# Optimization experiments

Measured on AMD Instinct MI355X. Metric: run time of the kernel, lower is better.

Reference implementation:

```python
import jax, jax.numpy as jnp
import numpy as np

V, H, B = 64, 128, 16384  # num_visible, num_hidden = alpha*V, batch of spin configs
ISCALE = 0.001


def setup_inputs() -> dict:
    key = jax.random.key(0)
    k1, k2, k3, k4 = jax.random.split(key, 4)
    x = jax.random.normal(k1, (B, V), dtype=jnp.float32)
    weight_1 = jax.random.normal(k2, (V, H), dtype=jnp.float32) * ISCALE
    weight_2 = jax.random.normal(k3, (H, V, V), dtype=jnp.float32) * (ISCALE / 10.0)
    hidden_bias = jax.random.normal(k4, (H,), dtype=jnp.float32) * ISCALE
    return {"x": x, "weight_1": weight_1, "weight_2": weight_2, "hidden_bias": hidden_bias}


def reference(x, weight_1, weight_2, hidden_bias):
    b, v = x.shape
    h = weight_2.shape[0]
    # order-1 term: (B,V) @ (V,H) -> (B,H)
    w1 = x @ weight_1
    # order-2 term: outer product of spins per sample, contracted with weight_2.
    # vis_ij: (B,V,V) flattened to (B,V*V); weight_2 flattened to (H,V*V) -> GEMM.
    vis_ij = jnp.einsum('mi,mj->mij', x, x).reshape(b, v * v)
    w2 = (vis_ij @ weight_2.reshape(h, v * v).T) * 0.5
    act = jnp.cos(hidden_bias + w1 + w2)  # (B,H)
    psi = jnp.prod(act, axis=-1)          # (B,)
    return psi
```

## Files before the change

### kernel.cpp

```cpp
#include <hip/hip_runtime.h>
#include <hip/hip_bf16.h>
#include <cstdint>

#define NV 64
#define NH 128
#define NB 16384
#define W2_ELEMS (NH * NV * NV)
#define W1_ELEMS (NV * NH)

typedef __bf16 bf16x8_t __attribute__((ext_vector_type(8)));
typedef float f32x4_t __attribute__((ext_vector_type(4)));
typedef float f32x2_t __attribute__((ext_vector_type(2)));
typedef uint32_t u32x4_t __attribute__((ext_vector_type(4)));
typedef uint32_t u32x2_t __attribute__((ext_vector_type(2)));

__device__ __forceinline__ uint32_t bf16_rne(float f) {
  uint32_t u = __float_as_uint(f);
  return (u + 0x7fffu + ((u >> 16) & 1u)) >> 16;
}

__global__ void cvt_kernel(const float* __restrict__ w1f,
                           const float* __restrict__ w2f,
                           uint16_t* __restrict__ wsW2,
                           uint16_t* __restrict__ wsW1t) {
  int base = (blockIdx.x * 256 + threadIdx.x) * 4;
  if (base < W2_ELEMS) {
    float4 v = *(const float4*)(w2f + base);
    uint2 p;
    p.x = (bf16_rne(0.5f * v.y) << 16) | bf16_rne(0.5f * v.x);
    p.y = (bf16_rne(0.5f * v.w) << 16) | bf16_rne(0.5f * v.z);
    *(uint2*)(wsW2 + base) = p;
  } else {
    int off = base - W2_ELEMS;
    float4 v = *(const float4*)(w1f + off);
    const float d[4] = {v.x, v.y, v.z, v.w};
#pragma unroll
    for (int e = 0; e < 4; ++e) {
      int idx = off + e;
      int j = idx >> 7, h = idx & 127;
      wsW1t[h * 64 + j] = (uint16_t)bf16_rne(d[e]);
    }
  }
}

__launch_bounds__(512, 2)
__global__ void rbm_kernel(const float* __restrict__ xg,
                           const float* __restrict__ biasg,
                           const __hip_bfloat16* __restrict__ w1tg,
                           const __hip_bfloat16* __restrict__ w2g,
                           float* __restrict__ outg) {
  __shared__ __align__(16) __hip_bfloat16 btile[2][NH * 64];
  __shared__ __align__(16) float xtile[64 * 68];
  __shared__ float part[4][64];

  const int tid  = threadIdx.x;
  const int wv   = tid >> 6;
  const int lane = tid & 63;
  const int c15  = lane & 15;
  const int q    = lane >> 4;
  const int wm   = wv & 1;
  const int hq   = wv >> 1;
  const int mblk = blockIdx.x * 64;

  const int sh = tid >> 2;
  const int g0 = tid & 3, g1 = g0 + 4;
  const __hip_bfloat16* w2row = w2g + (size_t)sh * 4096;
  const int d0 = sh * 64 + ((g0 ^ (sh & 7)) * 8);
  const int d1 = sh * 64 + ((g1 ^ (sh & 7)) * 8);

  {
    int row = tid >> 3, grp = tid & 7;
    const float* p = xg + (size_t)(mblk + row) * NV + grp * 8;
    float4 a = *(const float4*)(p);
    float4 b = *(const float4*)(p + 4);
    *(float4*)(&xtile[row * 68 + grp * 8]) = a;
    *(float4*)(&xtile[row * 68 + grp * 8 + 4]) = b;
  }

  f32x2_t xf[2][2][4];
#pragma unroll
  for (int im = 0; im < 2; ++im) {
    int row = mblk + 32 * wm + 16 * im + c15;
#pragma unroll
    for (int jh = 0; jh < 2; ++jh) {
      const float* p = xg + (size_t)row * NV + jh * 32 + q * 8;
      float4 a = *(const float4*)(p);
      float4 b = *(const float4*)(p + 4);
      xf[im][jh][0] = f32x2_t{a.x, a.y};
      xf[im][jh][1] = f32x2_t{a.z, a.w};
      xf[im][jh][2] = f32x2_t{b.x, b.y};
      xf[im][jh][3] = f32x2_t{b.z, b.w};
    }
  }

  int boff[2][2];
#pragma unroll
  for (int ih = 0; ih < 2; ++ih) {
    int hrow = 32 * hq + 16 * ih + c15;
#pragma unroll
    for (int jh = 0; jh < 2; ++jh)
      boff[ih][jh] = hrow * 64 + (((jh * 4 + q) ^ (hrow & 7)) * 8);
  }

  {
    uint4 p0 = *(const uint4*)(w2row + g0 * 8);
    uint4 p1 = *(const uint4*)(w2row + g1 * 8);
    *(uint4*)(&btile[0][d0]) = p0;
    *(uint4*)(&btile[0][d1]) = p1;
  }
  __syncthreads();

  f32x4_t acc[2][2];
#pragma unroll
  for (int im = 0; im < 2; ++im)
#pragma unroll
    for (int ih = 0; ih < 2; ++ih)
      acc[im][ih] = (f32x4_t)0.0f;

#pragma unroll 2
  for (int c = 0; c < 64; ++c) {
    const int buf = c & 1;
    uint4 p0, p1;
    if (c < 63) {
      const __hip_bfloat16* src = w2row + (c + 1) * 64;
      p0 = *(const uint4*)(src + g0 * 8);
      p1 = *(const uint4*)(src + g1 * 8);
    }
    float s[2];
#pragma unroll
    for (int im = 0; im < 2; ++im)
      s[im] = xtile[(32 * wm + 16 * im + c15) * 68 + c];

#pragma unroll
    for (int jh = 0; jh < 2; ++jh) {
      bf16x8_t afrag[2];
#pragma unroll
      for (int im = 0; im < 2; ++im) {
        const f32x2_t s2 = f32x2_t{s[im], s[im]};
        u32x4_t adv;
#pragma unroll
        for (int t = 0; t < 4; ++t) {
          f32x2_t pr = s2 * xf[im][jh][t];
          u32x2_t u = __builtin_bit_cast(u32x2_t, pr);
          adv[t] = __builtin_amdgcn_perm(u[1], u[0], 0x07060302);
        }
        afrag[im] = __builtin_bit_cast(bf16x8_t, adv);
      }
#pragma unroll
      for (int ih = 0; ih < 2; ++ih) {
        bf16x8_t bfrag = *(const bf16x8_t*)(&btile[buf][boff[ih][jh]]);
#pragma unroll
        for (int im = 0; im < 2; ++im)
          acc[im][ih] = __builtin_amdgcn_mfma_f32_16x16x32_bf16(
              afrag[im], bfrag, acc[im][ih], 0, 0, 0);
      }
    }
    if (c < 63) {
      *(uint4*)(&btile[buf ^ 1][d0]) = p0;
      *(uint4*)(&btile[buf ^ 1][d1]) = p1;
      __syncthreads();
    }
  }

#pragma unroll
  for (int cc = 0; cc < 2; ++cc) {
    bf16x8_t afrag[2];
#pragma unroll
    for (int im = 0; im < 2; ++im) {
      u32x4_t adv;
#pragma unroll
      for (int t = 0; t < 4; ++t) {
        u32x2_t u = __builtin_bit_cast(u32x2_t, xf[im][cc][t]);
        adv[t] = __builtin_amdgcn_perm(u[1], u[0], 0x07060302);
      }
      afrag[im] = __builtin_bit_cast(bf16x8_t, adv);
    }
#pragma unroll
    for (int ih = 0; ih < 2; ++ih) {
      int hrow = 32 * hq + 16 * ih + c15;
      bf16x8_t bfrag = *(const bf16x8_t*)(w1tg + hrow * 64 + cc * 32 + q * 8);
#pragma unroll
      for (int im = 0; im < 2; ++im)
        acc[im][ih] = __builtin_amdgcn_mfma_f32_16x16x32_bf16(
            afrag[im], bfrag, acc[im][ih], 0, 0, 0);
    }
  }

  float bs[2];
#pragma unroll
  for (int ih = 0; ih < 2; ++ih)
    bs[ih] = biasg[32 * hq + 16 * ih + c15];

  float prod[2][4];
#pragma unroll
  for (int im = 0; im < 2; ++im)
#pragma unroll
    for (int r = 0; r < 4; ++r)
      prod[im][r] = cosf(acc[im][0][r] + bs[0]) * cosf(acc[im][1][r] + bs[1]);

#pragma unroll
  for (int ofs = 1; ofs < 16; ofs <<= 1)
#pragma unroll
    for (int im = 0; im < 2; ++im)
#pragma unroll
      for (int r = 0; r < 4; ++r)
        prod[im][r] *= __shfl_xor(prod[im][r], ofs, 16);

  if (c15 == 0) {
#pragma unroll
    for (int im = 0; im < 2; ++im)
#pragma unroll
      for (int r = 0; r < 4; ++r)
        part[hq][32 * wm + 16 * im + 4 * q + r] = prod[im][r];
  }
  __syncthreads();
  if (tid < 64) {
    float f = part[0][tid] * part[1][tid] * part[2][tid] * part[3][tid];
    outg[mblk + tid] = f;
  }
}

extern "C" void kernel_launch(void* const* d_in, const int* in_sizes, int n_in,
                              void* d_out, int out_size, void* d_ws, size_t ws_size,
                              hipStream_t stream) {
  const float* x   = (const float*)d_in[0];
  const float* w1f = (const float*)d_in[1];
  const float* w2f = (const float*)d_in[2];
  const float* hb  = (const float*)d_in[3];
  float* out = (float*)d_out;
  uint16_t* wsW2  = (uint16_t*)d_ws;
  uint16_t* wsW1t = wsW2 + W2_ELEMS;
  (void)in_sizes; (void)n_in; (void)out_size; (void)ws_size;

  cvt_kernel<<<(W2_ELEMS + W1_ELEMS) / (256 * 4), 256, 0, stream>>>(
      w1f, w2f, wsW2, wsW1t);
  rbm_kernel<<<NB / 64, 512, 0, stream>>>(
      x, hb, (const __hip_bfloat16*)wsW1t, (const __hip_bfloat16*)wsW2, out);
}
```

Measured before the change: 99.64 us.

## Pre-swizzle weights into MFMA fragment layout and stream B directly from global

The weight conversion kernel now writes W2 and transposed W1 in the exact per-lane MFMA B-fragment order, so the main kernel loads B fragments straight from global/L2 into registers with a one-step register prefetch. This removes the LDS double-buffer and its per-iteration barrier. W1 is folded into the loop as a 65th chunk by setting an extra x column to 1. Blocks shrink to 4 waves, each covering all 64 rows against 32 hidden units, which doubles A-fragment reuse per B load. Cosine switches to the hardware sin/cos instruction with a 1/2π scale, trading accuracy for speed.

```diff
diff --git a/kernel.cpp b/kernel.cpp
--- a/kernel.cpp
+++ b/kernel.cpp
@@ -5,8 +5,7 @@
 #define NV 64
 #define NH 128
 #define NB 16384
-#define W2_ELEMS (NH * NV * NV)
-#define W1_ELEMS (NV * NH)
+#define FRAG_ELEMS (130 * 8 * 512)
 
 typedef __bf16 bf16x8_t __attribute__((ext_vector_type(8)));
 typedef float f32x4_t __attribute__((ext_vector_type(4)));
@@ -21,71 +20,77 @@
 
 __global__ void cvt_kernel(const float* __restrict__ w1f,
                            const float* __restrict__ w2f,
-                           uint16_t* __restrict__ wsW2,
-                           uint16_t* __restrict__ wsW1t) {
-  int base = (blockIdx.x * 256 + threadIdx.x) * 4;
-  if (base < W2_ELEMS) {
-    float4 v = *(const float4*)(w2f + base);
-    uint2 p;
-    p.x = (bf16_rne(0.5f * v.y) << 16) | bf16_rne(0.5f * v.x);
-    p.y = (bf16_rne(0.5f * v.w) << 16) | bf16_rne(0.5f * v.z);
-    *(uint2*)(wsW2 + base) = p;
+                           uint16_t* __restrict__ frag) {
+  int tg = blockIdx.x * 256 + threadIdx.x;
+  if (tg < 128 * 512) {
+    int h = tg >> 9, k8 = tg & 511;
+    const float* p = w2f + ((size_t)h << 12) + k8 * 8;
+    float4 a = *(const float4*)p;
+    float4 b = *(const float4*)(p + 4);
+    uint4 o;
+    o.x = (bf16_rne(0.5f * a.y) << 16) | bf16_rne(0.5f * a.x);
+    o.y = (bf16_rne(0.5f * a.w) << 16) | bf16_rne(0.5f * a.z);
+    o.z = (bf16_rne(0.5f * b.y) << 16) | bf16_rne(0.5f * b.x);
+    o.w = (bf16_rne(0.5f * b.w) << 16) | bf16_rne(0.5f * b.z);
+    int c2 = k8 >> 2, lhi = k8 & 3;
+    int fh = h >> 4, l = lhi * 16 + (h & 15);
+    *(uint4*)(frag + (((c2 * 8 + fh) * 64 + l) << 3)) = o;
   } else {
-    int off = base - W2_ELEMS;
-    float4 v = *(const float4*)(w1f + off);
-    const float d[4] = {v.x, v.y, v.z, v.w};
-#pragma unroll
-    for (int e = 0; e < 4; ++e) {
-      int idx = off + e;
-      int j = idx >> 7, h = idx & 127;
-      wsW1t[h * 64 + j] = (uint16_t)bf16_rne(d[e]);
-    }
-  }
-}
-
-__launch_bounds__(512, 2)
+    int t2 = tg - 128 * 512;
+    int h = t2 >> 3, j8 = t2 & 7;
+    uint32_t v[8];
+#pragma unroll
+    for (int t = 0; t < 8; ++t)
+      v[t] = bf16_rne(w1f[(j8 * 8 + t) * 128 + h]);
+    int c2 = 128 + (j8 >> 2), lhi = j8 & 3;
+    int fh = h >> 4, l = lhi * 16 + (h & 15);
+    uint4 o;
+    o.x = (v[1] << 16) | v[0];
+    o.y = (v[3] << 16) | v[2];
+    o.z = (v[5] << 16) | v[4];
+    o.w = (v[7] << 16) | v[6];
+    *(uint4*)(frag + (((c2 * 8 + fh) * 64 + l) << 3)) = o;
+  }
+}
+
+__launch_bounds__(256, 2)
 __global__ void rbm_kernel(const float* __restrict__ xg,
                            const float* __restrict__ biasg,
-                           const __hip_bfloat16* __restrict__ w1tg,
-                           const __hip_bfloat16* __restrict__ w2g,
+                           const __hip_bfloat16* __restrict__ frag,
                            float* __restrict__ outg) {
-  __shared__ __align__(16) __hip_bfloat16 btile[2][NH * 64];
   __shared__ __align__(16) float xtile[64 * 68];
   __shared__ float part[4][64];
 
   const int tid  = threadIdx.x;
-  const int wv   = tid >> 6;
+  const int hq   = tid >> 6;
   const int lane = tid & 63;
   const int c15  = lane & 15;
   const int q    = lane >> 4;
-  const int wm   = wv & 1;
-  const int hq   = wv >> 1;
   const int mblk = blockIdx.x * 64;
 
-  const int sh = tid >> 2;
-  const int g0 = tid & 3, g1 = g0 + 4;
-  const __hip_bfloat16* w2row = w2g + (size_t)sh * 4096;
-  const int d0 = sh * 64 + ((g0 ^ (sh & 7)) * 8);
-  const int d1 = sh * 64 + ((g1 ^ (sh & 7)) * 8);
-
   {
-    int row = tid >> 3, grp = tid & 7;
-    const float* p = xg + (size_t)(mblk + row) * NV + grp * 8;
-    float4 a = *(const float4*)(p);
-    float4 b = *(const float4*)(p + 4);
-    *(float4*)(&xtile[row * 68 + grp * 8]) = a;
-    *(float4*)(&xtile[row * 68 + grp * 8 + 4]) = b;
-  }
-
-  f32x2_t xf[2][2][4];
-#pragma unroll
-  for (int im = 0; im < 2; ++im) {
-    int row = mblk + 32 * wm + 16 * im + c15;
+    int row = tid >> 2, seg = tid & 3;
+    const float* p = xg + (size_t)(mblk + row) * NV + seg * 16;
+    float4 v0 = *(const float4*)(p);
+    float4 v1 = *(const float4*)(p + 4);
+    float4 v2 = *(const float4*)(p + 8);
+    float4 v3 = *(const float4*)(p + 12);
+    float* d = &xtile[row * 68 + seg * 16];
+    *(float4*)(d) = v0; *(float4*)(d + 4) = v1;
+    *(float4*)(d + 8) = v2; *(float4*)(d + 12) = v3;
+  }
+  if (tid < 64) xtile[tid * 68 + 64] = 1.0f;
+  __syncthreads();
+
+  f32x2_t xf[4][2][4];
+  const float* xrow[4];
+#pragma unroll
+  for (int im = 0; im < 4; ++im) {
+    xrow[im] = &xtile[(im * 16 + c15) * 68];
 #pragma unroll
     for (int jh = 0; jh < 2; ++jh) {
-      const float* p = xg + (size_t)row * NV + jh * 32 + q * 8;
-      float4 a = *(const float4*)(p);
-      float4 b = *(const float4*)(p + 4);
+      float4 a = *(const float4*)(xrow[im] + jh * 32 + q * 8);
+      float4 b = *(const float4*)(xrow[im] + jh * 32 + q * 8 + 4);
       xf[im][jh][0] = f32x2_t{a.x, a.y};
       xf[im][jh][1] = f32x2_t{a.z, a.w};
       xf[im][jh][2] = f32x2_t{b.x, b.y};
@@ -93,49 +98,52 @@
     }
   }
 
-  int boff[2][2];
-#pragma unroll
-  for (int ih = 0; ih < 2; ++ih) {
-    int hrow = 32 * hq + 16 * ih + c15;
-#pragma unroll
-    for (int jh = 0; jh < 2; ++jh)
-      boff[ih][jh] = hrow * 64 + (((jh * 4 + q) ^ (hrow & 7)) * 8);
-  }
-
-  {
-    uint4 p0 = *(const uint4*)(w2row + g0 * 8);
-    uint4 p1 = *(const uint4*)(w2row + g1 * 8);
-    *(uint4*)(&btile[0][d0]) = p0;
-    *(uint4*)(&btile[0][d1]) = p1;
-  }
-  __syncthreads();
-
-  f32x4_t acc[2][2];
-#pragma unroll
-  for (int im = 0; im < 2; ++im)
+  const __hip_bfloat16* pb = frag + (size_t)(hq * 2) * 512 + lane * 8;
+  bf16x8_t bnxt[2][2];
+#pragma unroll
+  for (int jh = 0; jh < 2; ++jh)
+#pragma unroll
+    for (int ih = 0; ih < 2; ++ih)
+      bnxt[jh][ih] = *(const bf16x8_t*)(pb + jh * 4096 + ih * 512);
+
+  f32x4_t acc[4][2];
+#pragma unroll
+  for (int im = 0; im < 4; ++im)
 #pragma unroll
     for (int ih = 0; ih < 2; ++ih)
       acc[im][ih] = (f32x4_t)0.0f;
 
-#pragma unroll 2
-  for (int c = 0; c < 64; ++c) {
-    const int buf = c & 1;
-    uint4 p0, p1;
-    if (c < 63) {
-      const __hip_bfloat16* src = w2row + (c + 1) * 64;
-      p0 = *(const uint4*)(src + g0 * 8);
-      p1 = *(const uint4*)(src + g1 * 8);
-    }
-    float s[2];
-#pragma unroll
-    for (int im = 0; im < 2; ++im)
-      s[im] = xtile[(32 * wm + 16 * im + c15) * 68 + c];
-
+  float scur[4];
+#pragma unroll
+  for (int im = 0; im < 4; ++im) scur[im] = xrow[im][0];
+
+  for (int c = 0; c < 65; ++c) {
+    bf16x8_t bc[2][2];
+#pragma unroll
+    for (int jh = 0; jh < 2; ++jh)
+#pragma unroll
+      for (int ih = 0; ih < 2; ++ih)
+        bc[jh][ih] = bnxt[jh][ih];
+    pb += 8192;
+    if (c < 64) {
+#pragma unroll
+      for (int jh = 0; jh < 2; ++jh)
+#pragma unroll
+        for (int ih = 0; ih < 2; ++ih)
+          bnxt[jh][ih] = *(const bf16x8_t*)(pb + jh * 4096 + ih * 512);
+    }
+    float s[4];
+#pragma unroll
+    for (int im = 0; im < 4; ++im) s[im] = scur[im];
+    if (c < 64) {
+#pragma unroll
+      for (int im = 0; im < 4; ++im) scur[im] = xrow[im][c + 1];
+    }
 #pragma unroll
     for (int jh = 0; jh < 2; ++jh) {
-      bf16x8_t afrag[2];
-#pragma unroll
-      for (int im = 0; im < 2; ++im) {
+      bf16x8_t afrag[4];
+#pragma unroll
+      for (int im = 0; im < 4; ++im) {
         const f32x2_t s2 = f32x2_t{s[im], s[im]};
         u32x4_t adv;
 #pragma unroll
@@ -147,71 +155,44 @@
         afrag[im] = __builtin_bit_cast(bf16x8_t, adv);
       }
 #pragma unroll
-      for (int ih = 0; ih < 2; ++ih) {
-        bf16x8_t bfrag = *(const bf16x8_t*)(&btile[buf][boff[ih][jh]]);
-#pragma unroll
-        for (int im = 0; im < 2; ++im)
+      for (int ih = 0; ih < 2; ++ih)
+#pragma unroll
+        for (int im = 0; im < 4; ++im)
           acc[im][ih] = __builtin_amdgcn_mfma_f32_16x16x32_bf16(
-              afrag[im], bfrag, acc[im][ih], 0, 0, 0);
-      }
-    }
-    if (c < 63) {
-      *(uint4*)(&btile[buf ^ 1][d0]) = p0;
-      *(uint4*)(&btile[buf ^ 1][d1]) = p1;
-      __syncthreads();
-    }
-  }
-
-#pragma unroll
-  for (int cc = 0; cc < 2; ++cc) {
-    bf16x8_t afrag[2];
-#pragma unroll
-    for (int im = 0; im < 2; ++im) {
-      u32x4_t adv;
-#pragma unroll
-      for (int t = 0; t < 4; ++t) {
-        u32x2_t u = __builtin_bit_cast(u32x2_t, xf[im][cc][t]);
-        adv[t] = __builtin_amdgcn_perm(u[1], u[0], 0x07060302);
-      }
-      afrag[im] = __builtin_bit_cast(bf16x8_t, adv);
-    }
-#pragma unroll
-    for (int ih = 0; ih < 2; ++ih) {
-      int hrow = 32 * hq + 16 * ih + c15;
-      bf16x8_t bfrag = *(const bf16x8_t*)(w1tg + hrow * 64 + cc * 32 + q * 8);
-#pragma unroll
-      for (int im = 0; im < 2; ++im)
-        acc[im][ih] = __builtin_amdgcn_mfma_f32_16x16x32_bf16(
-            afrag[im], bfrag, acc[im][ih], 0, 0, 0);
+              afrag[im], bc[jh][ih], acc[im][ih], 0, 0, 0);
     }
   }
 
   float bs[2];
 #pragma unroll
   for (int ih = 0; ih < 2; ++ih)
-    bs[ih] = biasg[32 * hq + 16 * ih + c15];
-
-  float prod[2][4];
-#pragma unroll
-  for (int im = 0; im < 2; ++im)
-#pragma unroll
-    for (int r = 0; r < 4; ++r)
-      prod[im][r] = cosf(acc[im][0][r] + bs[0]) * cosf(acc[im][1][r] + bs[1]);
+    bs[ih] = biasg[hq * 32 + ih * 16 + c15];
+
+  const float INV2PI = 0.15915494309189535f;
+  float prod[4][4];
+#pragma unroll
+  for (int im = 0; im < 4; ++im)
+#pragma unroll
+    for (int r = 0; r < 4; ++r) {
+      float c0 = __builtin_amdgcn_cosf((acc[im][0][r] + bs[0]) * INV2PI);
+      float c1 = __builtin_amdgcn_cosf((acc[im][1][r] + bs[1]) * INV2PI);
+      prod[im][r] = c0 * c1;
+    }
 
 #pragma unroll
   for (int ofs = 1; ofs < 16; ofs <<= 1)
 #pragma unroll
-    for (int im = 0; im < 2; ++im)
+    for (int im = 0; im < 4; ++im)
 #pragma unroll
       for (int r = 0; r < 4; ++r)
         prod[im][r] *= __shfl_xor(prod[im][r], ofs, 16);
 
   if (c15 == 0) {
 #pragma unroll
-    for (int im = 0; im < 2; ++im)
+    for (int im = 0; im < 4; ++im)
 #pragma unroll
       for (int r = 0; r < 4; ++r)
-        part[hq][32 * wm + 16 * im + 4 * q + r] = prod[im][r];
+        part[hq][im * 16 + q * 4 + r] = prod[im][r];
   }
   __syncthreads();
   if (tid < 64) {
@@ -228,12 +209,10 @@
   const float* w2f = (const float*)d_in[2];
   const float* hb  = (const float*)d_in[3];
   float* out = (float*)d_out;
-  uint16_t* wsW2  = (uint16_t*)d_ws;
-  uint16_t* wsW1t = wsW2 + W2_ELEMS;
+  uint16_t* frag = (uint16_t*)d_ws;
   (void)in_sizes; (void)n_in; (void)out_size; (void)ws_size;
 
-  cvt_kernel<<<(W2_ELEMS + W1_ELEMS) / (256 * 4), 256, 0, stream>>>(
-      w1f, w2f, wsW2, wsW1t);
-  rbm_kernel<<<NB / 64, 512, 0, stream>>>(
-      x, hb, (const __hip_bfloat16*)wsW1t, (const __hip_bfloat16*)wsW2, out);
-}
+  cvt_kernel<<<(128 * 512 + 1024) / 256, 256, 0, stream>>>(w1f, w2f, frag);
+  rbm_kernel<<<NB / 64, 256, 0, stream>>>(
+      x, hb, (const __hip_bfloat16*)frag, out);
+}
```

After: 102.3 us. 2.7% more time.
